# Optimization experiments

Hardware: AMD Instinct MI355X
Metric: run time of the kernel (lower is better)

Reference implementation:

```python
import jax, jax.numpy as jnp
import numpy as np

D_MODEL = 256
D_INNER = 512   # expand=2
D_STATE = 16
D_CONV = 4
DT_RANK = 16    # ceil(256/16)
N_LAYERS = 4
CITY = 300
BATCH = 32
EPS = 1e-5


def setup_inputs() -> dict:
    key = jax.random.key(0)
    ks = jax.random.split(key, 12)
    def rn(k, shape, scale=0.02):
        return (jax.random.normal(k, shape) * scale).astype(jnp.float32)
    inp = {}
    inp["coords"]   = jax.random.uniform(ks[0], (BATCH, CITY, 2), jnp.float32)
    inp["emb_W"]    = rn(ks[1], (D_MODEL, 2), 0.5)
    inp["emb_b"]    = jnp.zeros((D_MODEL,), jnp.float32)
    inp["ln_w"]     = jnp.ones((N_LAYERS, D_MODEL), jnp.float32)
    inp["ln_b"]     = jnp.zeros((N_LAYERS, D_MODEL), jnp.float32)
    inp["in_W"]     = rn(ks[2], (N_LAYERS, 2 * D_INNER, D_MODEL))
    inp["conv_W"]   = rn(ks[3], (N_LAYERS, D_INNER, D_CONV), 0.1)
    inp["conv_b"]   = jnp.zeros((N_LAYERS, D_INNER), jnp.float32)
    inp["xproj_W"]  = rn(ks[4], (N_LAYERS, DT_RANK + 2 * D_STATE, D_INNER))
    inp["dtproj_W"] = rn(ks[5], (N_LAYERS, D_INNER, DT_RANK), 0.1)
    inp["dtproj_b"] = rn(ks[6], (N_LAYERS, D_INNER), 0.1)
    # A initialized like mamba: S4D-real, A = -exp(A_log) with A in [1, 16]
    inp["A_log"]    = jnp.log(1.0 + jax.random.uniform(ks[7], (N_LAYERS, D_INNER, D_STATE), jnp.float32) * 15.0)
    inp["D_skip"]   = jnp.ones((N_LAYERS, D_INNER), jnp.float32)
    inp["out_W"]    = rn(ks[8], (N_LAYERS, D_MODEL, D_INNER))
    inp["normf_w"]  = jnp.ones((D_MODEL,), jnp.float32)
    inp["normf_b"]  = jnp.zeros((D_MODEL,), jnp.float32)
    inp["head_W"]   = rn(ks[9], (CITY, D_MODEL))
    return inp


def _layernorm(x, w, b):
    m = jnp.mean(x, axis=-1, keepdims=True)
    v = jnp.mean(jnp.square(x - m), axis=-1, keepdims=True)
    return (x - m) * jax.lax.rsqrt(v + EPS) * w + b


def _mamba_mixer(x, in_W, conv_W, conv_b, xproj_W, dtproj_W, dtproj_b, A_log, D_skip, out_W):
    # x: (B, L, d_model)
    Bsz = x.shape[0]
    xz = jnp.einsum('bld,ed->ble', x, in_W)            # (B, L, 2*d_inner)
    xi, z = jnp.split(xz, 2, axis=-1)                   # each (B, L, d_inner)
    # causal depthwise conv1d along L
    xc = jnp.swapaxes(xi, 1, 2)                         # (B, d_inner, L)
    xc = jax.lax.conv_general_dilated(
        xc, conv_W[:, None, :], (1,), [(D_CONV - 1, 0)],
        feature_group_count=D_INNER, dimension_numbers=('NCH', 'OIH', 'NCH'))
    xc = jax.nn.silu(jnp.swapaxes(xc, 1, 2) + conv_b)   # (B, L, d_inner)
    dbl = jnp.einsum('bld,ed->ble', xc, xproj_W)        # (B, L, dt_rank + 2*d_state)
    dt, Bm, Cm = jnp.split(dbl, [DT_RANK, DT_RANK + D_STATE], axis=-1)
    dt = jax.nn.softplus(jnp.einsum('blr,dr->bld', dt, dtproj_W) + dtproj_b)  # (B, L, d_inner)
    A = -jnp.exp(A_log)                                 # (d_inner, d_state)

    def step(h, inp):
        x_t, dt_t, B_t, C_t = inp                       # (B,dI),(B,dI),(B,dS),(B,dS)
        dA = jnp.exp(dt_t[..., None] * A)               # (B, dI, dS)
        h = dA * h + (dt_t * x_t)[..., None] * B_t[:, None, :]
        y = jnp.einsum('bds,bs->bd', h, C_t)
        return h, y

    h0 = jnp.zeros((Bsz, D_INNER, D_STATE), x.dtype)
    xs = (jnp.swapaxes(xc, 0, 1), jnp.swapaxes(dt, 0, 1),
          jnp.swapaxes(Bm, 0, 1), jnp.swapaxes(Cm, 0, 1))
    _, ys = jax.lax.scan(step, h0, xs)                  # ys: (L, B, d_inner)
    y = jnp.swapaxes(ys, 0, 1) + xc * D_skip
    y = y * jax.nn.silu(z)
    return jnp.einsum('ble,de->bld', y, out_W)          # (B, L, d_model)


def reference(coords, emb_W, emb_b, ln_w, ln_b, in_W, conv_W, conv_b, xproj_W,
              dtproj_W, dtproj_b, A_log, D_skip, out_W, normf_w, normf_b, head_W):
    x = jnp.einsum('blc,dc->bld', coords, emb_W) + emb_b
    residual = None
    for i in range(N_LAYERS):
        residual = x if residual is None else x + residual
        h = _layernorm(residual, ln_w[i], ln_b[i])
        x = _mamba_mixer(h, in_W[i], conv_W[i], conv_b[i], xproj_W[i],
                         dtproj_W[i], dtproj_b[i], A_log[i], D_skip[i], out_W[i])
    res = x + residual
    # final fused add + RMSNorm (is_rms_norm=True with LayerNorm weight/bias)
    rms = res * jax.lax.rsqrt(jnp.mean(res * res, axis=-1, keepdims=True) + EPS)
    out = rms * normf_w + normf_b
    logits = jnp.einsum('bld,cd->blc', out, head_W)     # (B, L, city_count)
    return logits
```

## Files before the change

### kernel.cpp

```cpp
#include <hip/hip_runtime.h>
#include <hip/hip_bf16.h>
#include <math.h>

#define D_MODEL 256
#define D_INNER 512
#define D_STATE 16
#define D_CONV 4
#define DT_RANK 16
#define N_LAYERS 4
#define CITY 300
#define BATCH 32
#define SEQ 300
#define NTOK (BATCH * SEQ)
#define NSEG 15
#define SEGLEN (SEQ / NSEG)

typedef __attribute__((ext_vector_type(8))) short short8v;
typedef __attribute__((ext_vector_type(4))) float f32x4;
typedef __attribute__((ext_vector_type(2))) float f32x2;

#define L2E_F 1.44269504088896340736f
#define LN2_F 0.69314718055994530942f

__device__ __forceinline__ float fexp2(float x) { return __builtin_amdgcn_exp2f(x); }
__device__ __forceinline__ float flog2(float x) { return __builtin_amdgcn_logf(x); }

__device__ __forceinline__ float fast_sig(float x) {
    return __builtin_amdgcn_rcpf(1.f + fexp2(-x * L2E_F));
}

__device__ __forceinline__ float softplus_f(float x) {
    float t = fexp2(-fabsf(x) * L2E_F);
    return fmaxf(x, 0.f) + flog2(1.f + t) * LN2_F;
}

__device__ __forceinline__ unsigned short f2b(float a) {
    __hip_bfloat16 h = __float2bfloat16(a);
    return *reinterpret_cast<unsigned short*>(&h);
}

__device__ __forceinline__ float b2f(unsigned short u) {
    unsigned int x = ((unsigned int)u) << 16;
    return __uint_as_float(x);
}

__device__ __forceinline__ float dtproj8(const float* rb, const f32x2* w2, float dtbv) {
    const f32x2* r2 = (const f32x2*)rb;
    f32x2 a0, a1, a2, a3;
    a0.x = dtbv; a0.y = 0.f;
    a1.x = 0.f; a1.y = 0.f;
    a2 = a1; a3 = a1;
    a0 = __builtin_elementwise_fma(r2[0], w2[0], a0);
    a1 = __builtin_elementwise_fma(r2[1], w2[1], a1);
    a2 = __builtin_elementwise_fma(r2[2], w2[2], a2);
    a3 = __builtin_elementwise_fma(r2[3], w2[3], a3);
    a0 = __builtin_elementwise_fma(r2[4], w2[4], a0);
    a1 = __builtin_elementwise_fma(r2[5], w2[5], a1);
    a2 = __builtin_elementwise_fma(r2[6], w2[6], a2);
    a3 = __builtin_elementwise_fma(r2[7], w2[7], a3);
    f32x2 s = (a0 + a1) + (a2 + a3);
    return s.x + s.y;
}

__global__ void cvt4_kernel(const float* __restrict__ s0, unsigned short* __restrict__ d0, int n0,
                            const float* __restrict__ s1, unsigned short* __restrict__ d1, int n1,
                            const float* __restrict__ s2, unsigned short* __restrict__ d2, int n2,
                            const float* __restrict__ s3, unsigned short* __restrict__ d3, int n3) {
    int stride = gridDim.x * blockDim.x;
    int tid = blockIdx.x * blockDim.x + threadIdx.x;
    for (int i = tid; i < n0 / 4; i += stride) {
        float4 v = ((const float4*)s0)[i];
        ushort4 o; o.x = f2b(v.x); o.y = f2b(v.y); o.z = f2b(v.z); o.w = f2b(v.w);
        ((ushort4*)d0)[i] = o;
    }
    for (int i = tid; i < n1 / 4; i += stride) {
        float4 v = ((const float4*)s1)[i];
        ushort4 o; o.x = f2b(v.x); o.y = f2b(v.y); o.z = f2b(v.z); o.w = f2b(v.w);
        ((ushort4*)d1)[i] = o;
    }
    for (int i = tid; i < n2 / 4; i += stride) {
        float4 v = ((const float4*)s2)[i];
        ushort4 o; o.x = f2b(v.x); o.y = f2b(v.y); o.z = f2b(v.z); o.w = f2b(v.w);
        ((ushort4*)d2)[i] = o;
    }
    for (int i = tid; i < n3 / 4; i += stride) {
        float4 v = ((const float4*)s3)[i];
        ushort4 o; o.x = f2b(v.x); o.y = f2b(v.y); o.z = f2b(v.z); o.w = f2b(v.w);
        ((ushort4*)d3)[i] = o;
    }
}

__global__ void embed_ln_kernel(const float* __restrict__ coords,
                                const float* __restrict__ eW,
                                const float* __restrict__ eb,
                                const float* __restrict__ w,
                                const float* __restrict__ b,
                                float* __restrict__ resid,
                                unsigned short* __restrict__ hb) {
    int t = blockIdx.x, d = threadIdx.x;
    float c0 = coords[t * 2 + 0];
    float c1 = coords[t * 2 + 1];
    float r = c0 * eW[d * 2 + 0] + c1 * eW[d * 2 + 1] + eb[d];
    resid[t * D_MODEL + d] = r;
    float s1 = r, s2 = r * r;
#pragma unroll
    for (int m = 1; m < 64; m <<= 1) {
        s1 += __shfl_xor(s1, m);
        s2 += __shfl_xor(s2, m);
    }
    __shared__ float p1[4], p2[4];
    if ((d & 63) == 0) { p1[d >> 6] = s1; p2[d >> 6] = s2; }
    __syncthreads();
    s1 = (p1[0] + p1[1]) + (p1[2] + p1[3]);
    s2 = (p2[0] + p2[1]) + (p2[2] + p2[3]);
    float mean = s1 * (1.f / D_MODEL);
    float var = s2 * (1.f / D_MODEL) - mean * mean;
    hb[t * D_MODEL + d] = f2b((r - mean) * rsqrtf(var + 1e-5f) * w[d] + b[d]);
}

template <int BM, int BN, bool GN, bool OB>
__global__ __launch_bounds__(256, 2) void gemm_mfma(const unsigned short* __restrict__ A,
                                                    const unsigned short* __restrict__ W,
                                                    void* __restrict__ C, int N, int K) {
    constexpr int TI = BM / 32;
    constexpr int TJ = BN / 32;
    __shared__ short Als[BM * 32];
    __shared__ short Bls[BN * 32];
    const int tid = threadIdx.x;
    const int lane = tid & 63, wid = tid >> 6;
    const int wr = wid >> 1, wc = wid & 1;
    const int t0 = blockIdx.x * BM, n0 = blockIdx.y * BN;
    f32x4 acc[TI][TJ] = {};

    for (int k0 = 0; k0 < K; k0 += 32) {
#pragma unroll
        for (int it = 0; it < BM / 64; ++it) {
            int s = tid + it * 256;
            int m = s >> 2, q = s & 3;
            uint4 p = *(const uint4*)(A + (size_t)(t0 + m) * K + k0 + q * 8);
            *(uint4*)&Als[(((m >> 4) * 4 + q) * 16 + (m & 15)) * 8] = p;
        }
#pragma unroll
        for (int it = 0; it < BN / 64; ++it) {
            int s = tid + it * 256;
            int n = s >> 2, q = s & 3;
            int nrow = n0 + n;
            uint4 p = make_uint4(0u, 0u, 0u, 0u);
            if (!GN || nrow < N)
                p = *(const uint4*)(W + (size_t)nrow * K + k0 + q * 8);
            *(uint4*)&Bls[(((n >> 4) * 4 + q) * 16 + (n & 15)) * 8] = p;
        }
        __syncthreads();
        short8v af[TI], bf[TJ];
#pragma unroll
        for (int i = 0; i < TI; i++)
            af[i] = *(const short8v*)&Als[(wr * TI + i) * 512 + lane * 8];
#pragma unroll
        for (int j = 0; j < TJ; j++)
            bf[j] = *(const short8v*)&Bls[(wc * TJ + j) * 512 + lane * 8];
#pragma unroll
        for (int i = 0; i < TI; i++)
#pragma unroll
            for (int j = 0; j < TJ; j++)
                acc[i][j] = __builtin_amdgcn_mfma_f32_16x16x32_bf16(
                    af[i], bf[j], acc[i][j], 0, 0, 0);
        __syncthreads();
    }
    const int rq = lane >> 4, cn = lane & 15;
#pragma unroll
    for (int i = 0; i < TI; i++) {
        int trow = t0 + wr * (BM / 2) + i * 16 + rq * 4;
#pragma unroll
        for (int j = 0; j < TJ; j++) {
            int ncol = n0 + wc * (BN / 2) + j * 16 + cn;
            if (!GN || ncol < N) {
#pragma unroll
                for (int reg = 0; reg < 4; reg++) {
                    if constexpr (OB)
                        ((unsigned short*)C)[(size_t)(trow + reg) * N + ncol] =
                            f2b(acc[i][j][reg]);
                    else
                        ((float*)C)[(size_t)(trow + reg) * N + ncol] = acc[i][j][reg];
                }
            }
        }
    }
}

__global__ __launch_bounds__(256, 2) void xproj_conv(
    const unsigned short* __restrict__ xzb,
    const float* __restrict__ cW, const float* __restrict__ cb,
    const unsigned short* __restrict__ W,
    unsigned short* __restrict__ xcb, float* __restrict__ dblo) {
    constexpr int TI = 2, TJ = 2;
    const int K = D_INNER, N = 48;
    __shared__ short Als[64 * 32];
    __shared__ short Bls[64 * 32];
    __shared__ float cwL[D_INNER * 4];
    __shared__ float cbL[D_INNER];
    const int tid = threadIdx.x;
    const int lane = tid & 63, wid = tid >> 6;
    const int wr = wid >> 1, wc = wid & 1;
    const int t0 = blockIdx.x * 64;

    for (int i = tid; i < D_INNER; i += 256) {
        ((float4*)cwL)[i] = ((const float4*)cW)[i];
        cbL[i] = cb[i];
    }
    __syncthreads();

    f32x4 acc[TI][TJ] = {};
    const int m = tid >> 2, q = tid & 3;
    const int t = t0 + m;
    const int l = t % SEQ;

    for (int k0 = 0; k0 < K; k0 += 32) {
        {
            const int ch0 = k0 + q * 8;
            const unsigned short* xr = xzb + (size_t)t * 1024 + ch0;
            uint4 u0 = make_uint4(0u, 0u, 0u, 0u), u1 = u0, u2 = u0, u3;
            if (l >= 3) u0 = *(const uint4*)(xr - 3 * 1024);
            if (l >= 2) u1 = *(const uint4*)(xr - 2 * 1024);
            if (l >= 1) u2 = *(const uint4*)(xr - 1 * 1024);
            u3 = *(const uint4*)xr;
            unsigned int ow0, ow1, ow2, ow3;
#pragma unroll
            for (int c2 = 0; c2 < 4; c2++) {
                unsigned int w0 = (c2 == 0) ? u0.x : (c2 == 1) ? u0.y : (c2 == 2) ? u0.z : u0.w;
                unsigned int w1 = (c2 == 0) ? u1.x : (c2 == 1) ? u1.y : (c2 == 2) ? u1.z : u1.w;
                unsigned int w2 = (c2 == 0) ? u2.x : (c2 == 1) ? u2.y : (c2 == 2) ? u2.z : u2.w;
                unsigned int w3 = (c2 == 0) ? u3.x : (c2 == 1) ? u3.y : (c2 == 2) ? u3.z : u3.w;
                int chA = ch0 + c2 * 2, chB = chA + 1;
                float4 wvA = *(const float4*)&cwL[chA * 4];
                float4 wvB = *(const float4*)&cwL[chB * 4];
                float aA = cbL[chA], aB = cbL[chB];
                aA = fmaf(b2f((unsigned short)(w0 & 0xffffu)), wvA.x, aA);
                aB = fmaf(b2f((unsigned short)(w0 >> 16)), wvB.x, aB);
                aA = fmaf(b2f((unsigned short)(w1 & 0xffffu)), wvA.y, aA);
                aB = fmaf(b2f((unsigned short)(w1 >> 16)), wvB.y, aB);
                aA = fmaf(b2f((unsigned short)(w2 & 0xffffu)), wvA.z, aA);
                aB = fmaf(b2f((unsigned short)(w2 >> 16)), wvB.z, aB);
                aA = fmaf(b2f((unsigned short)(w3 & 0xffffu)), wvA.w, aA);
                aB = fmaf(b2f((unsigned short)(w3 >> 16)), wvB.w, aB);
                aA = aA * fast_sig(aA);
                aB = aB * fast_sig(aB);
                unsigned int pk = (unsigned int)f2b(aA) | ((unsigned int)f2b(aB) << 16);
                if (c2 == 0) ow0 = pk; else if (c2 == 1) ow1 = pk; else if (c2 == 2) ow2 = pk; else ow3 = pk;
            }
            uint4 pk4 = make_uint4(ow0, ow1, ow2, ow3);
            *(uint4*)&Als[(((m >> 4) * 4 + q) * 16 + (m & 15)) * 8] = pk4;
            *(uint4*)(xcb + (size_t)t * 512 + ch0) = pk4;
        }
        {
            int n = tid >> 2;
            uint4 p = make_uint4(0u, 0u, 0u, 0u);
            if (n < N) p = *(const uint4*)(W + (size_t)n * K + k0 + q * 8);
            *(uint4*)&Bls[(((n >> 4) * 4 + q) * 16 + (n & 15)) * 8] = p;
        }
        __syncthreads();
        short8v af[TI], bf[TJ];
#pragma unroll
        for (int i = 0; i < TI; i++)
            af[i] = *(const short8v*)&Als[(wr * TI + i) * 512 + lane * 8];
#pragma unroll
        for (int j = 0; j < TJ; j++)
            bf[j] = *(const short8v*)&Bls[(wc * TJ + j) * 512 + lane * 8];
#pragma unroll
        for (int i = 0; i < TI; i++)
#pragma unroll
            for (int j = 0; j < TJ; j++)
                acc[i][j] = __builtin_amdgcn_mfma_f32_16x16x32_bf16(
                    af[i], bf[j], acc[i][j], 0, 0, 0);
        __syncthreads();
    }
    const int rq = lane >> 4, cn = lane & 15;
#pragma unroll
    for (int i = 0; i < TI; i++) {
        int trow = t0 + (wr * TI + i) * 16 + rq * 4;
#pragma unroll
        for (int j = 0; j < TJ; j++) {
            int ncol = wc * 32 + j * 16 + cn;
            if (ncol < N) {
#pragma unroll
                for (int reg = 0; reg < 4; reg++)
                    dblo[(size_t)(trow + reg) * N + ncol] = acc[i][j][reg];
            }
        }
    }
}

template <bool RMS>
__global__ __launch_bounds__(256, 2) void gemm_out_ln(const unsigned short* __restrict__ A,
                                                      const unsigned short* __restrict__ W,
                                                      float* __restrict__ resid,
                                                      const float* __restrict__ w,
                                                      const float* __restrict__ b,
                                                      unsigned short* __restrict__ hb) {
    constexpr int TI = 2, TJ = 8;
    const int K = D_INNER;
    __shared__ short Als[64 * 32];
    __shared__ short Bls[256 * 32];
    __shared__ float rs1[2][64], rs2[2][64];
    const int tid = threadIdx.x;
    const int lane = tid & 63, wid = tid >> 6;
    const int wr = wid >> 1, wc = wid & 1;
    const int t0 = blockIdx.x * 64;
    f32x4 acc[TI][TJ] = {};

    for (int k0 = 0; k0 < K; k0 += 32) {
        {
            int s = tid;
            int m = s >> 2, q = s & 3;
            uint4 p = *(const uint4*)(A + (size_t)(t0 + m) * K + k0 + q * 8);
            *(uint4*)&Als[(((m >> 4) * 4 + q) * 16 + (m & 15)) * 8] = p;
        }
#pragma unroll
        for (int it = 0; it < 4; ++it) {
            int s = tid + it * 256;
            int n = s >> 2, q = s & 3;
            uint4 p = *(const uint4*)(W + (size_t)n * K + k0 + q * 8);
            *(uint4*)&Bls[(((n >> 4) * 4 + q) * 16 + (n & 15)) * 8] = p;
        }
        __syncthreads();
        short8v af[TI], bf[TJ];
#pragma unroll
        for (int i = 0; i < TI; i++)
            af[i] = *(const short8v*)&Als[(wr * TI + i) * 512 + lane * 8];
#pragma unroll
        for (int j = 0; j < TJ; j++)
            bf[j] = *(const short8v*)&Bls[(wc * TJ + j) * 512 + lane * 8];
#pragma unroll
        for (int i = 0; i < TI; i++)
#pragma unroll
            for (int j = 0; j < TJ; j++)
                acc[i][j] = __builtin_amdgcn_mfma_f32_16x16x32_bf16(
                    af[i], bf[j], acc[i][j], 0, 0, 0);
        __syncthreads();
    }
    const int rq = lane >> 4, cn = lane & 15;
    float s1p[TI][4], s2p[TI][4];
#pragma unroll
    for (int i = 0; i < TI; i++) {
        int trow = t0 + wr * 32 + i * 16 + rq * 4;
#pragma unroll
        for (int reg = 0; reg < 4; reg++) { s1p[i][reg] = 0.f; s2p[i][reg] = 0.f; }
#pragma unroll
        for (int j = 0; j < TJ; j++) {
            int c = wc * 128 + j * 16 + cn;
#pragma unroll
            for (int reg = 0; reg < 4; reg++) {
                float rv = acc[i][j][reg] + resid[(size_t)(trow + reg) * D_MODEL + c];
                acc[i][j][reg] = rv;
                s1p[i][reg] += rv;
                s2p[i][reg] = fmaf(rv, rv, s2p[i][reg]);
            }
        }
    }
#pragma unroll
    for (int m = 1; m < 16; m <<= 1) {
#pragma unroll
        for (int i = 0; i < TI; i++)
#pragma unroll
            for (int reg = 0; reg < 4; reg++) {
                s1p[i][reg] += __shfl_xor(s1p[i][reg], m);
                s2p[i][reg] += __shfl_xor(s2p[i][reg], m);
            }
    }
    if (cn == 0) {
#pragma unroll
        for (int i = 0; i < TI; i++)
#pragma unroll
            for (int reg = 0; reg < 4; reg++) {
                int rloc = wr * 32 + i * 16 + rq * 4 + reg;
                rs1[wc][rloc] = s1p[i][reg];
                rs2[wc][rloc] = s2p[i][reg];
            }
    }
    __syncthreads();
    float wv[TJ], bv[TJ];
#pragma unroll
    for (int j = 0; j < TJ; j++) {
        int c = wc * 128 + j * 16 + cn;
        wv[j] = w[c];
        bv[j] = b[c];
    }
#pragma unroll
    for (int i = 0; i < TI; i++) {
        int trow = t0 + wr * 32 + i * 16 + rq * 4;
#pragma unroll
        for (int reg = 0; reg < 4; reg++) {
            int rloc = wr * 32 + i * 16 + rq * 4 + reg;
            float S1 = rs1[0][rloc] + rs1[1][rloc];
            float S2 = rs2[0][rloc] + rs2[1][rloc];
            float mean, rstd;
            if constexpr (RMS) {
                mean = 0.f;
                rstd = rsqrtf(S2 * (1.f / D_MODEL) + 1e-5f);
            } else {
                mean = S1 * (1.f / D_MODEL);
                float var = S2 * (1.f / D_MODEL) - mean * mean;
                rstd = rsqrtf(var + 1e-5f);
            }
#pragma unroll
            for (int j = 0; j < TJ; j++) {
                int c = wc * 128 + j * 16 + cn;
                float rv = acc[i][j][reg];
                hb[(size_t)(trow + reg) * D_MODEL + c] =
                    f2b((rv - mean) * rstd * wv[j] + bv[j]);
                if constexpr (!RMS)
                    resid[(size_t)(trow + reg) * D_MODEL + c] = rv;
            }
        }
    }
}

__global__ __launch_bounds__(960) void scan_block(
    const unsigned short* __restrict__ xcb, const float* __restrict__ dbl,
    const unsigned short* __restrict__ xzb,
    const float* __restrict__ A_log, const float* __restrict__ Dskip,
    const float* __restrict__ dtW, const float* __restrict__ dtb,
    float* __restrict__ dts, unsigned short* __restrict__ yb) {
    __shared__ float lh[NSEG * D_STATE * 64];
    __shared__ float lsd[NSEG * 64];
    const int b = blockIdx.x, dg = blockIdx.y;
    const int tid = threadIdx.x;
    const int lane = tid & 63;
    const int seg = __builtin_amdgcn_readfirstlane(tid >> 6);
    const int d = (dg << 6) + lane;
    f32x2 A2[8], w2[8];
#pragma unroll
    for (int s4 = 0; s4 < 4; s4++) {
        float4 v = *(const float4*)(A_log + (size_t)d * D_STATE + s4 * 4);
        f32x2 pa, pb;
        pa.x = -fexp2(v.x * L2E_F) * L2E_F;
        pa.y = -fexp2(v.y * L2E_F) * L2E_F;
        pb.x = -fexp2(v.z * L2E_F) * L2E_F;
        pb.y = -fexp2(v.w * L2E_F) * L2E_F;
        A2[s4 * 2 + 0] = pa;
        A2[s4 * 2 + 1] = pb;
        float4 w = *(const float4*)(dtW + (size_t)d * DT_RANK + s4 * 4);
        f32x2 qa, qb;
        qa.x = w.x; qa.y = w.y;
        qb.x = w.z; qb.y = w.w;
        w2[s4 * 2 + 0] = qa;
        w2[s4 * 2 + 1] = qb;
    }
    const float dtbv = dtb[d], dsk = Dskip[d];
    const size_t tb = (size_t)b * SEQ + (size_t)seg * SEGLEN;
    const float* __restrict__ dr = dbl + tb * 48;
    const unsigned short* __restrict__ xp = xcb + tb * 512 + d;
    const unsigned short* __restrict__ zp = xzb + tb * 1024 + 512 + d;
    float* __restrict__ dtp = dts + tb * 512 + d;
    unsigned short* __restrict__ yp = yb + tb * 512 + d;

    {
        f32x2 h2[8];
#pragma unroll
        for (int i = 0; i < 8; i++) { h2[i].x = 0.f; h2[i].y = 0.f; }
        float sdt = 0.f;
        float dbA[32], dbB[32];
#pragma unroll
        for (int i = 0; i < 8; i++) ((float4*)dbA)[i] = ((const float4*)dr)[i];
        float xv = b2f(xp[0]);
        for (int l = 0; l < SEGLEN; l += 2) {
            const float4* nr1 = (const float4*)(dr + (size_t)(l + 1) * 48);
#pragma unroll
            for (int i = 0; i < 8; i++) ((float4*)dbB)[i] = nr1[i];
            float xv1 = b2f(xp[(size_t)(l + 1) * 512]);
            {
                float acc = dtproj8(dbA, w2, dtbv);
                float dtt = softplus_f(acc);
                dtp[(size_t)l * 512] = dtt;
                sdt += dtt;
                float dtx = dtt * xv;
                f32x2 dtt2, dtx2;
                dtt2.x = dtt; dtt2.y = dtt;
                dtx2.x = dtx; dtx2.y = dtx;
                const f32x2* B2 = (const f32x2*)(dbA + 16);
#pragma unroll
                for (int i = 0; i < 8; i++) {
                    f32x2 g = dtt2 * A2[i];
                    f32x2 e;
                    e.x = fexp2(g.x);
                    e.y = fexp2(g.y);
                    h2[i] = __builtin_elementwise_fma(e, h2[i], dtx2 * B2[i]);
                }
            }
            const float4* nr2 = (const float4*)(dr + (size_t)(l + 2) * 48);
#pragma unroll
            for (int i = 0; i < 8; i++) ((float4*)dbA)[i] = nr2[i];
            float xv2 = b2f(xp[(size_t)(l + 2) * 512]);
            if (l + 1 < SEGLEN) {
                float acc = dtproj8(dbB, w2, dtbv);
                float dtt = softplus_f(acc);
                dtp[(size_t)(l + 1) * 512] = dtt;
                sdt += dtt;
                float dtx = dtt * xv1;
                f32x2 dtt2, dtx2;
                dtt2.x = dtt; dtt2.y = dtt;
                dtx2.x = dtx; dtx2.y = dtx;
                const f32x2* B2 = (const f32x2*)(dbB + 16);
#pragma unroll
                for (int i = 0; i < 8; i++) {
                    f32x2 g = dtt2 * A2[i];
                    f32x2 e;
                    e.x = fexp2(g.x);
                    e.y = fexp2(g.y);
                    h2[i] = __builtin_elementwise_fma(e, h2[i], dtx2 * B2[i]);
                }
            }
            xv = xv2;
        }
#pragma unroll
        for (int i = 0; i < 8; i++) {
            lh[(seg * D_STATE + 2 * i + 0) * 64 + lane] = h2[i].x;
            lh[(seg * D_STATE + 2 * i + 1) * 64 + lane] = h2[i].y;
        }
        lsd[seg * 64 + lane] = sdt;
    }
    __syncthreads();
    for (int it = tid; it < D_STATE * 64; it += 960) {
        int ch = it & 63, s = it >> 6;
        float As2 = -fexp2(A_log[(size_t)((dg << 6) + ch) * D_STATE + s] * L2E_F) * L2E_F;
        float hl[NSEG], sd[NSEG];
#pragma unroll
        for (int sg = 0; sg < NSEG; sg++) {
            hl[sg] = lh[(sg * D_STATE + s) * 64 + ch];
            sd[sg] = lsd[sg * 64 + ch];
        }
        float H = 0.f;
#pragma unroll
        for (int sg = 0; sg < NSEG; sg++) {
            lh[(sg * D_STATE + s) * 64 + ch] = H;
            H = fmaf(fexp2(As2 * sd[sg]), H, hl[sg]);
        }
    }
    __syncthreads();
    {
        f32x2 h2[8];
#pragma unroll
        for (int i = 0; i < 8; i++) {
            h2[i].x = lh[(seg * D_STATE + 2 * i + 0) * 64 + lane];
            h2[i].y = lh[(seg * D_STATE + 2 * i + 1) * 64 + lane];
        }
        float dbA[32], dbB[32];
#pragma unroll
        for (int i = 0; i < 8; i++) ((float4*)dbA)[i] = ((const float4*)(dr + 16))[i];
        float xv = b2f(xp[0]), zv = b2f(zp[0]);
        float dt0 = dtp[0];
        for (int l = 0; l < SEGLEN; l += 2) {
            const float4* nr1 = (const float4*)(dr + (size_t)(l + 1) * 48 + 16);
#pragma unroll
            for (int i = 0; i < 8; i++) ((float4*)dbB)[i] = nr1[i];
            float xv1 = b2f(xp[(size_t)(l + 1) * 512]);
            float zv1 = b2f(zp[(size_t)(l + 1) * 1024]);
            float dt1 = dtp[(size_t)(l + 1) * 512];
            {
                float dtt = dt0;
                float dtx = dtt * xv;
                f32x2 dtt2, dtx2;
                dtt2.x = dtt; dtt2.y = dtt;
                dtx2.x = dtx; dtx2.y = dtx;
                f32x2 ya, yc;
                ya.x = 0.f; ya.y = 0.f; yc = ya;
                const f32x2* B2 = (const f32x2*)dbA;
                const f32x2* C2 = (const f32x2*)(dbA + 16);
#pragma unroll
                for (int i = 0; i < 8; i++) {
                    f32x2 g = dtt2 * A2[i];
                    f32x2 e;
                    e.x = fexp2(g.x);
                    e.y = fexp2(g.y);
                    h2[i] = __builtin_elementwise_fma(e, h2[i], dtx2 * B2[i]);
                    if (i & 1)
                        yc = __builtin_elementwise_fma(h2[i], C2[i], yc);
                    else
                        ya = __builtin_elementwise_fma(h2[i], C2[i], ya);
                }
                f32x2 ys = ya + yc;
                float y = ys.x + ys.y;
                yp[(size_t)l * 512] = f2b((y + xv * dsk) * (zv * fast_sig(zv)));
            }
            const float4* nr2 = (const float4*)(dr + (size_t)(l + 2) * 48 + 16);
#pragma unroll
            for (int i = 0; i < 8; i++) ((float4*)dbA)[i] = nr2[i];
            float xv2 = b2f(xp[(size_t)(l + 2) * 512]);
            float zv2 = b2f(zp[(size_t)(l + 2) * 1024]);
            float dt2 = dtp[(size_t)(l + 2) * 512];
            if (l + 1 < SEGLEN) {
                float dtt = dt1;
                float dtx = dtt * xv1;
                f32x2 dtt2, dtx2;
                dtt2.x = dtt; dtt2.y = dtt;
                dtx2.x = dtx; dtx2.y = dtx;
                f32x2 ya, yc;
                ya.x = 0.f; ya.y = 0.f; yc = ya;
                const f32x2* B2 = (const f32x2*)dbB;
                const f32x2* C2 = (const f32x2*)(dbB + 16);
#pragma unroll
                for (int i = 0; i < 8; i++) {
                    f32x2 g = dtt2 * A2[i];
                    f32x2 e;
                    e.x = fexp2(g.x);
                    e.y = fexp2(g.y);
                    h2[i] = __builtin_elementwise_fma(e, h2[i], dtx2 * B2[i]);
                    if (i & 1)
                        yc = __builtin_elementwise_fma(h2[i], C2[i], yc);
                    else
                        ya = __builtin_elementwise_fma(h2[i], C2[i], ya);
                }
                f32x2 ys = ya + yc;
                float y = ys.x + ys.y;
                yp[(size_t)(l + 1) * 512] = f2b((y + xv1 * dsk) * (zv1 * fast_sig(zv1)));
            }
            xv = xv2; zv = zv2; dt0 = dt2;
        }
    }
}

extern "C" void kernel_launch(void* const* d_in, const int* in_sizes, int n_in,
                              void* d_out, int out_size, void* d_ws, size_t ws_size,
                              hipStream_t stream) {
    const float* coords   = (const float*)d_in[0];
    const float* emb_W    = (const float*)d_in[1];
    const float* emb_b    = (const float*)d_in[2];
    const float* ln_w     = (const float*)d_in[3];
    const float* ln_b     = (const float*)d_in[4];
    const float* in_W     = (const float*)d_in[5];
    const float* conv_W   = (const float*)d_in[6];
    const float* conv_b   = (const float*)d_in[7];
    const float* xproj_W  = (const float*)d_in[8];
    const float* dtproj_W = (const float*)d_in[9];
    const float* dtproj_b = (const float*)d_in[10];
    const float* A_log    = (const float*)d_in[11];
    const float* D_skip   = (const float*)d_in[12];
    const float* out_W    = (const float*)d_in[13];
    const float* normf_w  = (const float*)d_in[14];
    const float* normf_b  = (const float*)d_in[15];
    const float* head_W   = (const float*)d_in[16];
    float* out = (float*)d_out;

    const int T = NTOK;
    float* resid = (float*)d_ws;
    float* dbl   = resid + (size_t)T * D_MODEL;
    float* dts   = dbl + (size_t)T * 48;
    unsigned short* hb     = (unsigned short*)(dts + (size_t)T * D_INNER);
    unsigned short* xzb    = hb + (size_t)T * D_MODEL;
    unsigned short* xcb    = xzb + (size_t)T * 2 * D_INNER;
    unsigned short* yb     = xcb + (size_t)T * D_INNER;
    unsigned short* wb_in  = yb + (size_t)T * D_INNER;
    unsigned short* wb_xp  = wb_in + (size_t)N_LAYERS * 2 * D_INNER * D_MODEL;
    unsigned short* wb_out = wb_xp + (size_t)N_LAYERS * 48 * D_INNER;
    unsigned short* wb_hd  = wb_out + (size_t)N_LAYERS * D_MODEL * D_INNER;

    cvt4_kernel<<<256, 256, 0, stream>>>(
        in_W, wb_in, N_LAYERS * 2 * D_INNER * D_MODEL,
        xproj_W, wb_xp, N_LAYERS * 48 * D_INNER,
        out_W, wb_out, N_LAYERS * D_MODEL * D_INNER,
        head_W, wb_hd, CITY * D_MODEL);

    embed_ln_kernel<<<T, D_MODEL, 0, stream>>>(coords, emb_W, emb_b, ln_w, ln_b, resid, hb);

    for (int i = 0; i < N_LAYERS; i++) {
        gemm_mfma<128, 128, false, true><<<dim3(T / 128, 8), 256, 0, stream>>>(
            hb, wb_in + (size_t)i * 2 * D_INNER * D_MODEL, xzb, 2 * D_INNER, D_MODEL);
        xproj_conv<<<T / 64, 256, 0, stream>>>(
            xzb, conv_W + i * D_INNER * D_CONV, conv_b + i * D_INNER,
            wb_xp + (size_t)i * 48 * D_INNER, xcb, dbl);
        scan_block<<<dim3(BATCH, 8), 960, 0, stream>>>(
            xcb, dbl, xzb, A_log + (size_t)i * D_INNER * D_STATE, D_skip + i * D_INNER,
            dtproj_W + (size_t)i * D_INNER * DT_RANK, dtproj_b + i * D_INNER, dts, yb);
        if (i < N_LAYERS - 1)
            gemm_out_ln<false><<<T / 64, 256, 0, stream>>>(
                yb, wb_out + (size_t)i * D_MODEL * D_INNER, resid,
                ln_w + (i + 1) * D_MODEL, ln_b + (i + 1) * D_MODEL, hb);
        else
            gemm_out_ln<true><<<T / 64, 256, 0, stream>>>(
                yb, wb_out + (size_t)i * D_MODEL * D_INNER, resid,
                normf_w, normf_b, hb);
    }

    gemm_mfma<64, 64, true, false><<<dim3(T / 64, 5), 256, 0, stream>>>(
        hb, wb_hd, out, CITY, D_MODEL);
}
```

Measured before the change: 457.3 us.

## Fuse embedding+LayerNorm into first in-proj GEMM and head GEMM into final out-proj

Removes the standalone embedding/LayerNorm kernel by computing the embedding and normalization in-block inside the first in_proj GEMM, keeping the normalized tile in shared memory. The final out_proj+RMSNorm kernel now also runs the head projection from a shared-memory tile, removing the separate head GEMM launch and the hb round trip. Each in_proj block recomputes the embedding for its 128 rows across 8 column blocks. The head fusion adds 32KB of LDS per block and serializes five head chunks per block, which may reduce occupancy and parallelism for the last stage.

```diff
diff --git a/kernel.cpp b/kernel.cpp
--- a/kernel.cpp
+++ b/kernel.cpp
@@ -90,34 +90,6 @@
     }
 }
 
-__global__ void embed_ln_kernel(const float* __restrict__ coords,
-                                const float* __restrict__ eW,
-                                const float* __restrict__ eb,
-                                const float* __restrict__ w,
-                                const float* __restrict__ b,
-                                float* __restrict__ resid,
-                                unsigned short* __restrict__ hb) {
-    int t = blockIdx.x, d = threadIdx.x;
-    float c0 = coords[t * 2 + 0];
-    float c1 = coords[t * 2 + 1];
-    float r = c0 * eW[d * 2 + 0] + c1 * eW[d * 2 + 1] + eb[d];
-    resid[t * D_MODEL + d] = r;
-    float s1 = r, s2 = r * r;
-#pragma unroll
-    for (int m = 1; m < 64; m <<= 1) {
-        s1 += __shfl_xor(s1, m);
-        s2 += __shfl_xor(s2, m);
-    }
-    __shared__ float p1[4], p2[4];
-    if ((d & 63) == 0) { p1[d >> 6] = s1; p2[d >> 6] = s2; }
-    __syncthreads();
-    s1 = (p1[0] + p1[1]) + (p1[2] + p1[3]);
-    s2 = (p2[0] + p2[1]) + (p2[2] + p2[3]);
-    float mean = s1 * (1.f / D_MODEL);
-    float var = s2 * (1.f / D_MODEL) - mean * mean;
-    hb[t * D_MODEL + d] = f2b((r - mean) * rsqrtf(var + 1e-5f) * w[d] + b[d]);
-}
-
 template <int BM, int BN, bool GN, bool OB>
 __global__ __launch_bounds__(256, 2) void gemm_mfma(const unsigned short* __restrict__ A,
                                                     const unsigned short* __restrict__ W,
@@ -183,6 +155,101 @@
                         ((float*)C)[(size_t)(trow + reg) * N + ncol] = acc[i][j][reg];
                 }
             }
+        }
+    }
+}
+
+__global__ __launch_bounds__(256, 2) void in_proj_embed(
+    const float* __restrict__ coords, const float* __restrict__ eW,
+    const float* __restrict__ eb, const float* __restrict__ lw,
+    const float* __restrict__ lb, float* __restrict__ resid,
+    const unsigned short* __restrict__ W, unsigned short* __restrict__ xzb) {
+    constexpr int TI = 4, TJ = 4;
+    const int K = D_MODEL, N = 2 * D_INNER;
+    __shared__ short hbL[128 * 256];
+    __shared__ short Bls[128 * 32];
+    const int tid = threadIdx.x;
+    const int lane = tid & 63, wid = tid >> 6;
+    const int wr = wid >> 1, wc = wid & 1;
+    const int t0 = blockIdx.x * 128, n0 = blockIdx.y * 128;
+    const int by = blockIdx.y;
+
+    {
+        const int d0 = lane * 4;
+        const int slab = d0 >> 5, q = (d0 & 31) >> 3, r = d0 & 7;
+        float4 lw4 = ((const float4*)lw)[lane];
+        float4 lb4 = ((const float4*)lb)[lane];
+        float4 eb4 = ((const float4*)eb)[lane];
+        float4 f4a = ((const float4*)eW)[d0 >> 1];
+        float4 f4b = ((const float4*)eW)[(d0 >> 1) + 1];
+        for (int p = 0; p < 32; ++p) {
+            int m = p * 4 + wid;
+            int t = t0 + m;
+            float c0 = coords[t * 2 + 0];
+            float c1 = coords[t * 2 + 1];
+            float e0 = fmaf(c1, f4a.y, fmaf(c0, f4a.x, eb4.x));
+            float e1 = fmaf(c1, f4a.w, fmaf(c0, f4a.z, eb4.y));
+            float e2 = fmaf(c1, f4b.y, fmaf(c0, f4b.x, eb4.z));
+            float e3 = fmaf(c1, f4b.w, fmaf(c0, f4b.z, eb4.w));
+            float s1 = (e0 + e1) + (e2 + e3);
+            float s2 = fmaf(e0, e0, fmaf(e1, e1, fmaf(e2, e2, e3 * e3)));
+#pragma unroll
+            for (int msk = 1; msk < 64; msk <<= 1) {
+                s1 += __shfl_xor(s1, msk);
+                s2 += __shfl_xor(s2, msk);
+            }
+            float mean = s1 * (1.f / D_MODEL);
+            float var = s2 * (1.f / D_MODEL) - mean * mean;
+            float rstd = rsqrtf(var + 1e-5f);
+            ushort4 pk;
+            pk.x = f2b((e0 - mean) * rstd * lw4.x + lb4.x);
+            pk.y = f2b((e1 - mean) * rstd * lw4.y + lb4.y);
+            pk.z = f2b((e2 - mean) * rstd * lw4.z + lb4.z);
+            pk.w = f2b((e3 - mean) * rstd * lw4.w + lb4.w);
+            *(ushort4*)&hbL[slab * 4096 + (((m >> 4) * 4 + q) * 16 + (m & 15)) * 8 + r] = pk;
+            if (by == 0) {
+                float4 rv; rv.x = e0; rv.y = e1; rv.z = e2; rv.w = e3;
+                *(float4*)(resid + (size_t)t * D_MODEL + d0) = rv;
+            }
+        }
+    }
+    __syncthreads();
+
+    f32x4 acc[TI][TJ] = {};
+    for (int k0 = 0; k0 < K; k0 += 32) {
+#pragma unroll
+        for (int it = 0; it < 2; ++it) {
+            int s = tid + it * 256;
+            int n = s >> 2, q = s & 3;
+            uint4 p = *(const uint4*)(W + (size_t)(n0 + n) * K + k0 + q * 8);
+            *(uint4*)&Bls[(((n >> 4) * 4 + q) * 16 + (n & 15)) * 8] = p;
+        }
+        __syncthreads();
+        short8v af[TI], bf[TJ];
+#pragma unroll
+        for (int i = 0; i < TI; i++)
+            af[i] = *(const short8v*)&hbL[(k0 >> 5) * 4096 + (wr * TI + i) * 512 + lane * 8];
+#pragma unroll
+        for (int j = 0; j < TJ; j++)
+            bf[j] = *(const short8v*)&Bls[(wc * TJ + j) * 512 + lane * 8];
+#pragma unroll
+        for (int i = 0; i < TI; i++)
+#pragma unroll
+            for (int j = 0; j < TJ; j++)
+                acc[i][j] = __builtin_amdgcn_mfma_f32_16x16x32_bf16(
+                    af[i], bf[j], acc[i][j], 0, 0, 0);
+        __syncthreads();
+    }
+    const int rq = lane >> 4, cn = lane & 15;
+#pragma unroll
+    for (int i = 0; i < TI; i++) {
+        int trow = t0 + wr * 64 + i * 16 + rq * 4;
+#pragma unroll
+        for (int j = 0; j < TJ; j++) {
+            int ncol = n0 + wc * 64 + j * 16 + cn;
+#pragma unroll
+            for (int reg = 0; reg < 4; reg++)
+                xzb[(size_t)(trow + reg) * N + ncol] = f2b(acc[i][j][reg]);
         }
     }
 }
@@ -289,18 +356,21 @@
     }
 }
 
-template <bool RMS>
+template <bool RMS, bool HEAD>
 __global__ __launch_bounds__(256, 2) void gemm_out_ln(const unsigned short* __restrict__ A,
                                                       const unsigned short* __restrict__ W,
                                                       float* __restrict__ resid,
                                                       const float* __restrict__ w,
                                                       const float* __restrict__ b,
-                                                      unsigned short* __restrict__ hb) {
+                                                      unsigned short* __restrict__ hb,
+                                                      const unsigned short* __restrict__ hW,
+                                                      float* __restrict__ outp) {
     constexpr int TI = 2, TJ = 8;
     const int K = D_INNER;
     __shared__ short Als[64 * 32];
     __shared__ short Bls[256 * 32];
     __shared__ float rs1[2][64], rs2[2][64];
+    __shared__ short hN[HEAD ? 64 * 256 : 1];
     const int tid = threadIdx.x;
     const int lane = tid & 63, wid = tid >> 6;
     const int wr = wid >> 1, wc = wid & 1;
@@ -405,10 +475,56 @@
             for (int j = 0; j < TJ; j++) {
                 int c = wc * 128 + j * 16 + cn;
                 float rv = acc[i][j][reg];
-                hb[(size_t)(trow + reg) * D_MODEL + c] =
-                    f2b((rv - mean) * rstd * wv[j] + bv[j]);
+                unsigned short nv = f2b((rv - mean) * rstd * wv[j] + bv[j]);
+                if constexpr (HEAD) {
+                    int mrow = wr * 32 + i * 16 + rq * 4 + reg;
+                    hN[(c >> 5) * 2048 + (((mrow >> 4) * 4 + ((c & 31) >> 3)) * 16 + (mrow & 15)) * 8 + (c & 7)] = (short)nv;
+                } else {
+                    hb[(size_t)(trow + reg) * D_MODEL + c] = nv;
+                }
                 if constexpr (!RMS)
                     resid[(size_t)(trow + reg) * D_MODEL + c] = rv;
+            }
+        }
+    }
+    if constexpr (HEAD) {
+        __syncthreads();
+        for (int nch = 0; nch < 5; ++nch) {
+            f32x4 acc2[2][2] = {};
+            for (int k0 = 0; k0 < D_MODEL; k0 += 32) {
+                int n = tid >> 2, q = tid & 3;
+                int nrow = nch * 64 + n;
+                uint4 p = make_uint4(0u, 0u, 0u, 0u);
+                if (nrow < CITY) p = *(const uint4*)(hW + (size_t)nrow * D_MODEL + k0 + q * 8);
+                *(uint4*)&Bls[(((n >> 4) * 4 + q) * 16 + (n & 15)) * 8] = p;
+                __syncthreads();
+                short8v af2[2], bf2[2];
+#pragma unroll
+                for (int i = 0; i < 2; i++)
+                    af2[i] = *(const short8v*)&hN[(k0 >> 5) * 2048 + (wr * 2 + i) * 512 + lane * 8];
+#pragma unroll
+                for (int j = 0; j < 2; j++)
+                    bf2[j] = *(const short8v*)&Bls[(wc * 2 + j) * 512 + lane * 8];
+#pragma unroll
+                for (int i = 0; i < 2; i++)
+#pragma unroll
+                    for (int j = 0; j < 2; j++)
+                        acc2[i][j] = __builtin_amdgcn_mfma_f32_16x16x32_bf16(
+                            af2[i], bf2[j], acc2[i][j], 0, 0, 0);
+                __syncthreads();
+            }
+#pragma unroll
+            for (int i = 0; i < 2; i++) {
+                int trow = t0 + (wr * 2 + i) * 16 + rq * 4;
+#pragma unroll
+                for (int j = 0; j < 2; j++) {
+                    int ncol = nch * 64 + wc * 32 + j * 16 + cn;
+                    if (ncol < CITY) {
+#pragma unroll
+                        for (int reg = 0; reg < 4; reg++)
+                            outp[(size_t)(trow + reg) * CITY + ncol] = acc2[i][j][reg];
+                    }
+                }
             }
         }
     }
@@ -659,11 +775,13 @@
         out_W, wb_out, N_LAYERS * D_MODEL * D_INNER,
         head_W, wb_hd, CITY * D_MODEL);
 
-    embed_ln_kernel<<<T, D_MODEL, 0, stream>>>(coords, emb_W, emb_b, ln_w, ln_b, resid, hb);
-
     for (int i = 0; i < N_LAYERS; i++) {
-        gemm_mfma<128, 128, false, true><<<dim3(T / 128, 8), 256, 0, stream>>>(
-            hb, wb_in + (size_t)i * 2 * D_INNER * D_MODEL, xzb, 2 * D_INNER, D_MODEL);
+        if (i == 0)
+            in_proj_embed<<<dim3(T / 128, 8), 256, 0, stream>>>(
+                coords, emb_W, emb_b, ln_w, ln_b, resid, wb_in, xzb);
+        else
+            gemm_mfma<128, 128, false, true><<<dim3(T / 128, 8), 256, 0, stream>>>(
+                hb, wb_in + (size_t)i * 2 * D_INNER * D_MODEL, xzb, 2 * D_INNER, D_MODEL);
         xproj_conv<<<T / 64, 256, 0, stream>>>(
             xzb, conv_W + i * D_INNER * D_CONV, conv_b + i * D_INNER,
             wb_xp + (size_t)i * 48 * D_INNER, xcb, dbl);
@@ -671,15 +789,12 @@
             xcb, dbl, xzb, A_log + (size_t)i * D_INNER * D_STATE, D_skip + i * D_INNER,
             dtproj_W + (size_t)i * D_INNER * DT_RANK, dtproj_b + i * D_INNER, dts, yb);
         if (i < N_LAYERS - 1)
-            gemm_out_ln<false><<<T / 64, 256, 0, stream>>>(
+            gemm_out_ln<false, false><<<T / 64, 256, 0, stream>>>(
                 yb, wb_out + (size_t)i * D_MODEL * D_INNER, resid,
-                ln_w + (i + 1) * D_MODEL, ln_b + (i + 1) * D_MODEL, hb);
+                ln_w + (i + 1) * D_MODEL, ln_b + (i + 1) * D_MODEL, hb, nullptr, nullptr);
         else
-            gemm_out_ln<true><<<T / 64, 256, 0, stream>>>(
+            gemm_out_ln<true, true><<<T / 64, 256, 0, stream>>>(
                 yb, wb_out + (size_t)i * D_MODEL * D_INNER, resid,
-                normf_w, normf_b, hb);
-    }
-
-    gemm_mfma<64, 64, true, false><<<dim3(T / 64, 5), 256, 0, stream>>>(
-        hb, wb_hd, out, CITY, D_MODEL);
-}
+                normf_w, normf_b, hb, wb_hd, out);
+    }
+}
```

New measurement: 478.1 us. 1.05x slower.

## Fuse head projection GEMM into final out-projection RMSNorm kernel

Applied to the files above, without the earlier changes.

The final layer's out-projection+RMSNorm kernel now stores the normalized bf16 rows in shared memory in MFMA-fragment layout and computes the 300-column head GEMM itself in five 64-column chunks. The separate head GEMM launch and the global write/read of the normalized activations are removed. In exchange it adds 32KB of shared memory per block, which may lower occupancy, and the head GEMM runs with only T/64 blocks, less parallelism than the old 5x grid. The head weights are also re-read per block with a sync per k-step.

```diff
diff --git a/kernel.cpp b/kernel.cpp
--- a/kernel.cpp
+++ b/kernel.cpp
@@ -289,18 +289,21 @@
     }
 }
 
-template <bool RMS>
+template <bool RMS, bool HEAD>
 __global__ __launch_bounds__(256, 2) void gemm_out_ln(const unsigned short* __restrict__ A,
                                                       const unsigned short* __restrict__ W,
                                                       float* __restrict__ resid,
                                                       const float* __restrict__ w,
                                                       const float* __restrict__ b,
-                                                      unsigned short* __restrict__ hb) {
+                                                      unsigned short* __restrict__ hb,
+                                                      const unsigned short* __restrict__ hW,
+                                                      float* __restrict__ outp) {
     constexpr int TI = 2, TJ = 8;
     const int K = D_INNER;
     __shared__ short Als[64 * 32];
     __shared__ short Bls[256 * 32];
     __shared__ float rs1[2][64], rs2[2][64];
+    __shared__ short hN[HEAD ? 64 * 256 : 1];
     const int tid = threadIdx.x;
     const int lane = tid & 63, wid = tid >> 6;
     const int wr = wid >> 1, wc = wid & 1;
@@ -405,10 +408,56 @@
             for (int j = 0; j < TJ; j++) {
                 int c = wc * 128 + j * 16 + cn;
                 float rv = acc[i][j][reg];
-                hb[(size_t)(trow + reg) * D_MODEL + c] =
-                    f2b((rv - mean) * rstd * wv[j] + bv[j]);
+                unsigned short nv = f2b((rv - mean) * rstd * wv[j] + bv[j]);
+                if constexpr (HEAD) {
+                    int mrow = wr * 32 + i * 16 + rq * 4 + reg;
+                    hN[(c >> 5) * 2048 + (((mrow >> 4) * 4 + ((c & 31) >> 3)) * 16 + (mrow & 15)) * 8 + (c & 7)] = (short)nv;
+                } else {
+                    hb[(size_t)(trow + reg) * D_MODEL + c] = nv;
+                }
                 if constexpr (!RMS)
                     resid[(size_t)(trow + reg) * D_MODEL + c] = rv;
+            }
+        }
+    }
+    if constexpr (HEAD) {
+        __syncthreads();
+        for (int nch = 0; nch < 5; ++nch) {
+            f32x4 acc2[2][2] = {};
+            for (int k0 = 0; k0 < D_MODEL; k0 += 32) {
+                int n = tid >> 2, q = tid & 3;
+                int nrow = nch * 64 + n;
+                uint4 p = make_uint4(0u, 0u, 0u, 0u);
+                if (nrow < CITY) p = *(const uint4*)(hW + (size_t)nrow * D_MODEL + k0 + q * 8);
+                *(uint4*)&Bls[(((n >> 4) * 4 + q) * 16 + (n & 15)) * 8] = p;
+                __syncthreads();
+                short8v af2[2], bf2[2];
+#pragma unroll
+                for (int i = 0; i < 2; i++)
+                    af2[i] = *(const short8v*)&hN[(k0 >> 5) * 2048 + (wr * 2 + i) * 512 + lane * 8];
+#pragma unroll
+                for (int j = 0; j < 2; j++)
+                    bf2[j] = *(const short8v*)&Bls[(wc * 2 + j) * 512 + lane * 8];
+#pragma unroll
+                for (int i = 0; i < 2; i++)
+#pragma unroll
+                    for (int j = 0; j < 2; j++)
+                        acc2[i][j] = __builtin_amdgcn_mfma_f32_16x16x32_bf16(
+                            af2[i], bf2[j], acc2[i][j], 0, 0, 0);
+                __syncthreads();
+            }
+#pragma unroll
+            for (int i = 0; i < 2; i++) {
+                int trow = t0 + (wr * 2 + i) * 16 + rq * 4;
+#pragma unroll
+                for (int j = 0; j < 2; j++) {
+                    int ncol = nch * 64 + wc * 32 + j * 16 + cn;
+                    if (ncol < CITY) {
+#pragma unroll
+                        for (int reg = 0; reg < 4; reg++)
+                            outp[(size_t)(trow + reg) * CITY + ncol] = acc2[i][j][reg];
+                    }
+                }
             }
         }
     }
@@ -671,15 +720,12 @@
             xcb, dbl, xzb, A_log + (size_t)i * D_INNER * D_STATE, D_skip + i * D_INNER,
             dtproj_W + (size_t)i * D_INNER * DT_RANK, dtproj_b + i * D_INNER, dts, yb);
         if (i < N_LAYERS - 1)
-            gemm_out_ln<false><<<T / 64, 256, 0, stream>>>(
+            gemm_out_ln<false, false><<<T / 64, 256, 0, stream>>>(
                 yb, wb_out + (size_t)i * D_MODEL * D_INNER, resid,
-                ln_w + (i + 1) * D_MODEL, ln_b + (i + 1) * D_MODEL, hb);
+                ln_w + (i + 1) * D_MODEL, ln_b + (i + 1) * D_MODEL, hb, nullptr, nullptr);
         else
-            gemm_out_ln<true><<<T / 64, 256, 0, stream>>>(
+            gemm_out_ln<true, true><<<T / 64, 256, 0, stream>>>(
                 yb, wb_out + (size_t)i * D_MODEL * D_INNER, resid,
-                normf_w, normf_b, hb);
-    }
-
-    gemm_mfma<64, 64, true, false><<<dim3(T / 64, 5), 256, 0, stream>>>(
-        hb, wb_hd, out, CITY, D_MODEL);
-}
+                normf_w, normf_b, hb, wb_hd, out);
+    }
+}
```

After: 463.2 us. About the same (+1.3%).
